# Optimization experiments

Hardware: AMD Instinct MI355X
Metric: run time of the kernel (lower is better)

## Reference

```python
import jax, jax.numpy as jnp
import numpy as np

IN_CH = 32
OUT_CH = 32
HIDDEN = 32  # edge/angle MLP hidden width


def setup_inputs() -> dict:
    key = jax.random.key(0)
    ks = jax.random.split(key, 13)
    N, E, A = 50000, 200000, 400000
    s = 0.1
    return {
        "x": jax.random.normal(ks[0], (N, IN_CH), dtype=jnp.float32),
        "edge_index": jax.random.randint(ks[1], (2, E), 0, N),
        "edge_attr": jax.random.uniform(ks[2], (E, 1), dtype=jnp.float32),
        "angle_index": jax.random.randint(ks[3], (3, A), 0, N),
        "angles": jax.random.uniform(ks[4], (A, 1), dtype=jnp.float32),
        # edge_mlp: Linear(1,32) -> ReLU -> Linear(32, in*out)
        "eW1": jax.random.normal(ks[5], (1, HIDDEN), dtype=jnp.float32) * s,
        "eb1": jax.random.normal(ks[6], (HIDDEN,), dtype=jnp.float32) * s,
        "eW2": jax.random.normal(ks[7], (HIDDEN, IN_CH * OUT_CH), dtype=jnp.float32) * s,
        "eb2": jax.random.normal(ks[8], (IN_CH * OUT_CH,), dtype=jnp.float32) * s,
        # angle_mlp: Linear(1,32) -> ReLU -> Linear(32, out)
        "aW1": jax.random.normal(ks[9], (1, HIDDEN), dtype=jnp.float32) * s,
        "ab1": jax.random.normal(ks[10], (HIDDEN,), dtype=jnp.float32) * s,
        "aW2": jax.random.normal(ks[11], (HIDDEN, OUT_CH), dtype=jnp.float32) * s,
        "ab2": jax.random.normal(ks[12], (OUT_CH,), dtype=jnp.float32) * s,
    }


def reference(x, edge_index, edge_attr, angle_index, angles,
              eW1, eb1, eW2, eb2, aW1, ab1, aW2, ab2):
    N = x.shape[0]
    row, col = edge_index[0], edge_index[1]
    # per-edge weight matrices from edge MLP: (E, in, out)
    h = jax.nn.relu(edge_attr @ eW1 + eb1)
    edge_w = (h @ eW2 + eb2).reshape(-1, IN_CH, OUT_CH)
    # gather source node features, apply per-edge matrix (bmm)
    msg = jnp.einsum('ei,eio->eo', x[col], edge_w)  # (E, out)
    agg = jax.ops.segment_sum(msg, row, num_segments=N)
    # angle branch: scatter angle features onto center node j
    j = angle_index[1]
    angle_feat = jax.nn.relu(angles @ aW1 + ab1) @ aW2 + ab2  # (A, out)
    agg = agg + jax.ops.segment_sum(angle_feat, j, num_segments=N)
    return agg
```

## Files before the change

### kernel.cpp

```cpp
#include <hip/hip_runtime.h>
#include <hip/hip_bf16.h>
#include <stdint.h>

#define IC 32
#define OC 32
#define HID 32

#define PBIN 16
#define TSH 44
#define TSCALE 1048576.0f

typedef __attribute__((ext_vector_type(8))) _Float16 half8;
typedef __attribute__((ext_vector_type(4))) float f32x4;
typedef unsigned long long u64;

static __device__ __forceinline__ _Float16 f2h(float f) { return (_Float16)f; }

__global__ void zero_kernel(float* __restrict__ out, int n) {
    int i = (blockIdx.x * blockDim.x + threadIdx.x) * 4;
    if (i + 3 < n) {
        *(float4*)(out + i) = make_float4(0.f, 0.f, 0.f, 0.f);
    } else {
        for (int k = i; k < n; ++k) out[k] = 0.f;
    }
}

__global__ __launch_bounds__(256) void angle_scatter(
    const float* __restrict__ angles, const int* __restrict__ angle_index,
    const float* __restrict__ aW1, const float* __restrict__ ab1,
    u64* __restrict__ cells, int A)
{
    float w1[HID], b1[HID];
#pragma unroll
    for (int k = 0; k < HID; ++k) { w1[k] = aW1[k]; b1[k] = ab1[k]; }

    int i0 = blockIdx.x * blockDim.x + threadIdx.x;
    int stride = gridDim.x * blockDim.x;
    for (int a = i0; a < A; a += stride) {
        const float t = angles[a];
        const int j = angle_index[A + a];
        int c = 0, c0 = 0;
#pragma unroll
        for (int k = 0; k < HID; ++k) {
            const bool pos = w1[k] > 0.f;
            const bool on  = fmaf(t, w1[k], b1[k]) > 0.f;
            const bool on0 = b1[k] > 0.f;
            c  += (pos ? on  : !on ) ? 1 : 0;
            c0 += (pos ? on0 : !on0) ? 1 : 0;
        }
        const int cc = c - c0;
        if ((unsigned)cc < (unsigned)PBIN) {
            const u64 enc = ((u64)1 << TSH) | (u64)(unsigned)(t * TSCALE);
            atomicAdd(cells + (size_t)j * PBIN + cc, enc);
        }
    }
}

__global__ __launch_bounds__(256) void angle_gather(
    float* __restrict__ out,
    const float* __restrict__ aW1, const float* __restrict__ ab1,
    const float* __restrict__ aW2, const float* __restrict__ ab2,
    int N)
{
    const int lane = threadIdx.x & 63;
    const int q    = lane >> 4;
    const int l15  = lane & 15;
    const int wib  = threadIdx.x >> 6;
    const int base = (blockIdx.x * 4 + wib) * 16;
    if (base >= N) return;

    float w1s[8], b1s[8];
    int c0 = 0, c1 = 0;
#pragma unroll
    for (int k = 0; k < HID; ++k) {
        const float w = aW1[k], b = ab1[k];
        const bool pos = w > 0.f;
        const bool f0 = pos ? (b > 0.f) : !(b > 0.f);
        const bool f1 = pos ? ((w + b) > 0.f) : !((w + b) > 0.f);
        c0 += f0 ? 1 : 0;
        c1 += f1 ? 1 : 0;
        if ((k >> 3) == q) { w1s[k & 7] = w; b1s[k & 7] = b; }
    }
    int npc = c1 - c0 + 1;
    if (npc > PBIN) npc = PBIN;

    half8 Bf0, Bf1;
#pragma unroll
    for (int j = 0; j < 8; ++j) {
        Bf0[j] = f2h(aW2[(q * 8 + j) * OC + l15]);
        Bf1[j] = f2h(aW2[(q * 8 + j) * OC + 16 + l15]);
    }
    const float bias0 = ab2[l15];
    const float bias1 = ab2[16 + l15];

    const int jn = base + l15;
    const bool vn = (jn < N);
    const u64* cj = (const u64*)out + (size_t)(vn ? jn : 0) * PBIN;
    float g[8] = {0.f, 0.f, 0.f, 0.f, 0.f, 0.f, 0.f, 0.f};
    float tot = 0.f;
    for (int cc = 0; cc < npc; ++cc) {
        const u64 v = vn ? cj[cc] : 0;
        if (v) {
            const float n  = (float)(unsigned)(v >> TSH);
            const float ts = (float)(v & (((u64)1 << TSH) - 1)) * (1.f / TSCALE);
            const float tb = ts / n;
#pragma unroll
            for (int k = 0; k < 8; ++k) {
                float h = fmaf(tb, w1s[k], b1s[k]);
                h = h > 0.f ? h : 0.f;
                g[k] = fmaf(n, h, g[k]);
            }
            tot += n;
        }
    }
    half8 a;
#pragma unroll
    for (int k = 0; k < 8; ++k) a[k] = f2h(g[k]);

    f32x4 acc0 = {0.f, 0.f, 0.f, 0.f};
    f32x4 acc1 = {0.f, 0.f, 0.f, 0.f};
    acc0 = __builtin_amdgcn_mfma_f32_16x16x32_f16(a, Bf0, acc0, 0, 0, 0);
    acc1 = __builtin_amdgcn_mfma_f32_16x16x32_f16(a, Bf1, acc1, 0, 0, 0);

#pragma unroll
    for (int r = 0; r < 4; ++r) {
        const int node = base + q * 4 + r;
        const float tr = __shfl(tot, q * 4 + r, 64);
        if (node < N) {
            out[(size_t)node * OC + l15]      = fmaf(tr, bias0, acc0[r]);
            out[(size_t)node * OC + 16 + l15] = fmaf(tr, bias1, acc1[r]);
        }
    }
}

__global__ __launch_bounds__(256) void angle_fixup(
    const float* __restrict__ angles, const int* __restrict__ angle_index,
    const float* __restrict__ aW1, const float* __restrict__ ab1,
    const float* __restrict__ aW2, const float* __restrict__ ab2,
    float* __restrict__ out, int A)
{
    float w1[HID], b1[HID];
#pragma unroll
    for (int k = 0; k < HID; ++k) { w1[k] = aW1[k]; b1[k] = ab1[k]; }

    int c0 = 0, c1 = 0;
#pragma unroll
    for (int k = 0; k < HID; ++k) {
        const bool pos = w1[k] > 0.f;
        const bool f0 = pos ? (b1[k] > 0.f) : !(b1[k] > 0.f);
        const bool f1 = pos ? ((w1[k] + b1[k]) > 0.f) : !((w1[k] + b1[k]) > 0.f);
        c0 += f0 ? 1 : 0;
        c1 += f1 ? 1 : 0;
    }
    if (c1 - c0 + 1 <= PBIN) return;

    int i0 = blockIdx.x * blockDim.x + threadIdx.x;
    int stride = gridDim.x * blockDim.x;
    for (int a = i0; a < A; a += stride) {
        const float t = angles[a];
        const int j = angle_index[A + a];
        int c = 0;
#pragma unroll
        for (int k = 0; k < HID; ++k) {
            const bool pos = w1[k] > 0.f;
            const bool on  = fmaf(t, w1[k], b1[k]) > 0.f;
            c += (pos ? on : !on) ? 1 : 0;
        }
        if (c - c0 >= PBIN) {
            float h[HID];
#pragma unroll
            for (int k = 0; k < HID; ++k) {
                float v = fmaf(t, w1[k], b1[k]);
                h[k] = v > 0.f ? v : 0.f;
            }
            for (int o = 0; o < OC; ++o) {
                float s = ab2[o];
#pragma unroll
                for (int k = 0; k < HID; ++k) s = fmaf(h[k], aW2[k * OC + o], s);
                unsafeAtomicAdd(out + (size_t)j * OC + o, s);
            }
        }
    }
}

__global__ __launch_bounds__(256) void edge_kernel(
    const float* __restrict__ x, const int* __restrict__ edge_index,
    const float* __restrict__ edge_attr,
    const float* __restrict__ eW1, const float* __restrict__ eb1,
    const float* __restrict__ eW2, const float* __restrict__ eb2,
    float* __restrict__ out, int E)
{
    const int tid   = threadIdx.x;
    const int lane  = tid & 63;
    const int gwave = blockIdx.x * 4 + (tid >> 6);
    const int ot    = gwave & 1;
    const int tile0 = gwave >> 1;
    const int tstride = (gridDim.x * 4) >> 1;
    const int q     = lane >> 4;
    const int l15   = lane & 15;
    const int ocol  = ot * 16 + l15;

    half8 Bf[33];
#pragma unroll
    for (int s = 0; s < 32; ++s) {
        half8 b;
#pragma unroll
        for (int j = 0; j < 8; ++j)
            b[j] = f2h(eW2[s * 1024 + (q * 8 + j) * 32 + ocol]);
        Bf[s] = b;
    }
    {
        half8 b;
#pragma unroll
        for (int j = 0; j < 8; ++j)
            b[j] = f2h(eb2[(q * 8 + j) * 32 + ocol]);
        Bf[32] = b;
    }

    const int numTiles = (E + 15) >> 4;

    for (int tile = tile0; tile < numTiles; tile += 2 * tstride) {
        const int tA = tile;
        const int tB = tile + tstride;
        const bool hasB = (tB < numTiles);

        const int eA  = (tA << 4) + l15;
        const bool va = (eA < E);
        const int eAc = va ? eA : 0;
        const float ta = va ? edge_attr[eAc] : 0.f;
        const int colA = va ? edge_index[E + eAc] : 0;

        const int eB  = (tB << 4) + l15;
        const bool vb = hasB && (eB < E);
        const int eBc = vb ? eB : 0;
        const float tb = vb ? edge_attr[eBc] : 0.f;
        const int colB = vb ? edge_index[E + eBc] : 0;

        const float* xpA = x + (size_t)colA * IC + q * 8;
        const float4 xloA = *(const float4*)(xpA);
        const float4 xhiA = *(const float4*)(xpA + 4);
        const float* xpB = x + (size_t)colB * IC + q * 8;
        const float4 xloB = *(const float4*)(xpB);
        const float4 xhiB = *(const float4*)(xpB + 4);

        int dstsA[4], dstsB[4];
        const int ebaseA = (tA << 4) + q * 4;
        const int ebaseB = (tB << 4) + q * 4;
#pragma unroll
        for (int r = 0; r < 4; ++r) {
            const int erA = ebaseA + r;
            dstsA[r] = (erA < E) ? edge_index[erA] : -1;
            const int erB = ebaseB + r;
            dstsB[r] = (hasB && erB < E) ? edge_index[erB] : -1;
        }

        half8 xhA, xhB;
        xhA[0] = f2h(xloA.x); xhA[1] = f2h(xloA.y);
        xhA[2] = f2h(xloA.z); xhA[3] = f2h(xloA.w);
        xhA[4] = f2h(xhiA.x); xhA[5] = f2h(xhiA.y);
        xhA[6] = f2h(xhiA.z); xhA[7] = f2h(xhiA.w);
        xhB[0] = f2h(xloB.x); xhB[1] = f2h(xloB.y);
        xhB[2] = f2h(xloB.z); xhB[3] = f2h(xloB.w);
        xhB[4] = f2h(xhiB.x); xhB[5] = f2h(xhiB.y);
        xhB[6] = f2h(xhiB.z); xhB[7] = f2h(xhiB.w);

        f32x4 accA = {0.f, 0.f, 0.f, 0.f};
        f32x4 accB = {0.f, 0.f, 0.f, 0.f};
#pragma unroll
        for (int s = 0; s < 32; ++s) {
            const float w1s = eW1[s], b1s = eb1[s];
            float hsA = fmaf(ta, w1s, b1s);
            hsA = hsA > 0.f ? hsA : 0.f;
            float hsB = fmaf(tb, w1s, b1s);
            hsB = hsB > 0.f ? hsB : 0.f;
            const _Float16 hA = f2h(hsA);
            const _Float16 hB = f2h(hsB);
            half8 hvA = {hA, hA, hA, hA, hA, hA, hA, hA};
            half8 hvB = {hB, hB, hB, hB, hB, hB, hB, hB};
            half8 aA = xhA * hvA;
            half8 aB = xhB * hvB;
            accA = __builtin_amdgcn_mfma_f32_16x16x32_f16(aA, Bf[s], accA, 0, 0, 0);
            accB = __builtin_amdgcn_mfma_f32_16x16x32_f16(aB, Bf[s], accB, 0, 0, 0);
        }
        {
            accA = __builtin_amdgcn_mfma_f32_16x16x32_f16(xhA, Bf[32], accA, 0, 0, 0);
            accB = __builtin_amdgcn_mfma_f32_16x16x32_f16(xhB, Bf[32], accB, 0, 0, 0);
        }

#pragma unroll
        for (int r = 0; r < 4; ++r) {
            if (dstsA[r] >= 0)
                unsafeAtomicAdd(out + (size_t)dstsA[r] * OC + ocol, accA[r]);
        }
#pragma unroll
        for (int r = 0; r < 4; ++r) {
            if (dstsB[r] >= 0)
                unsafeAtomicAdd(out + (size_t)dstsB[r] * OC + ocol, accB[r]);
        }
    }
}

extern "C" void kernel_launch(void* const* d_in, const int* in_sizes, int n_in,
                              void* d_out, int out_size, void* d_ws, size_t ws_size,
                              hipStream_t stream)
{
    const float* x          = (const float*)d_in[0];
    const int*   edge_index = (const int*)d_in[1];
    const float* edge_attr  = (const float*)d_in[2];
    const int*   angle_index= (const int*)d_in[3];
    const float* angles     = (const float*)d_in[4];
    const float* eW1        = (const float*)d_in[5];
    const float* eb1        = (const float*)d_in[6];
    const float* eW2        = (const float*)d_in[7];
    const float* eb2        = (const float*)d_in[8];
    const float* aW1        = (const float*)d_in[9];
    const float* ab1        = (const float*)d_in[10];
    const float* aW2        = (const float*)d_in[11];
    const float* ab2        = (const float*)d_in[12];
    float* out = (float*)d_out;
    (void)d_ws; (void)ws_size;

    const int E = in_sizes[1] / 2;
    const int A = in_sizes[3] / 3;
    const int N = in_sizes[0] / IC;

    const int zblocks = (out_size / 4 + 255) / 256;
    zero_kernel<<<zblocks, 256, 0, stream>>>(out, out_size);

    const int sblocks = (A + 255) / 256;
    angle_scatter<<<sblocks, 256, 0, stream>>>(angles, angle_index,
                                               aW1, ab1, (u64*)out, A);

    const int gblocks = (N + 63) / 64;
    angle_gather<<<gblocks, 256, 0, stream>>>(out, aW1, ab1, aW2, ab2, N);

    angle_fixup<<<sblocks, 256, 0, stream>>>(angles, angle_index,
                                             aW1, ab1, aW2, ab2, out, A);

    edge_kernel<<<512, 256, 0, stream>>>(x, edge_index, edge_attr,
                                         eW1, eb1, eW2, eb2, out, E);
}
```

Baseline: 166.8 us.

## Use piecewise-linear edge MLP decomposition with precomputed per-piece weight matrices

A setup kernel finds the ReLU breakpoints of the edge and angle hidden layers inside (0,1) and folds each linear piece into two fp16 32x32 matrices (constant part and slope part). The edge kernel stages these in LDS and runs two MFMAs per piece, masked to the edge's piece, instead of 33 MFMAs per tile. It also grows blocks to 512 threads, and the angle scatter now uses the precomputed knots. A scalar fixup kernel covers the case with more pieces than the table holds. This assumes attributes lie in [0,1) and adds a setup launch plus a data-dependent loop length.

```diff
diff --git a/kernel.cpp b/kernel.cpp
--- a/kernel.cpp
+++ b/kernel.cpp
@@ -10,11 +10,90 @@
 #define TSH 44
 #define TSCALE 1048576.0f
 
+#define PBE 12
+
 typedef __attribute__((ext_vector_type(8))) _Float16 half8;
 typedef __attribute__((ext_vector_type(4))) float f32x4;
 typedef unsigned long long u64;
 
 static __device__ __forceinline__ _Float16 f2h(float f) { return (_Float16)f; }
+
+__device__ __align__(16) _Float16 g_MK[PBE * 2 * 32 * 32];
+__device__ float g_ekn[16];
+__device__ float g_akn[16];
+__device__ int   g_npc[2];
+
+__global__ __launch_bounds__(256) void setup_kernel(
+    const float* __restrict__ eW1, const float* __restrict__ eb1,
+    const float* __restrict__ eW2, const float* __restrict__ eb2,
+    const float* __restrict__ aW1, const float* __restrict__ ab1)
+{
+    __shared__ float ts_s[32];
+    __shared__ int   rk_s[32];
+    __shared__ int   re_s[32];
+    const int tid = threadIdx.x;
+
+    if (blockIdx.x == 0 && tid < 16) { g_ekn[tid] = 1e30f; g_akn[tid] = 1e30f; }
+
+    if (tid < 32) {
+        const int k = tid;
+        const float w = eW1[k], b = eb1[k];
+        const float ts = -b / w;
+        const bool re = (w != 0.f) && (ts > 0.f) && (ts < 1.f);
+        int rk = 0;
+        for (int k2 = 0; k2 < 32; ++k2) {
+            const float w2 = eW1[k2], b2 = eb1[k2];
+            const float t2 = -b2 / w2;
+            const bool re2 = (w2 != 0.f) && (t2 > 0.f) && (t2 < 1.f);
+            rk += (re2 && (t2 < ts || (t2 == ts && k2 < k))) ? 1 : 0;
+        }
+        ts_s[k] = ts; rk_s[k] = rk; re_s[k] = re ? 1 : 0;
+    }
+    __syncthreads();
+
+    if (blockIdx.x == 0) {
+        if (tid < 32) {
+            if (re_s[tid]) g_ekn[rk_s[tid]] = ts_s[tid];
+            if (tid == 0) {
+                int n = 0;
+                for (int k = 0; k < 32; ++k) n += re_s[k];
+                g_npc[0] = n + 1;
+            }
+        } else if (tid < 64) {
+            const int k = tid - 32;
+            const float w = aW1[k], b = ab1[k];
+            const float ts = -b / w;
+            const bool re = (w != 0.f) && (ts > 0.f) && (ts < 1.f);
+            int rk = 0, nre = 0;
+            for (int k2 = 0; k2 < 32; ++k2) {
+                const float w2 = aW1[k2], b2 = ab1[k2];
+                const float t2 = -b2 / w2;
+                const bool re2 = (w2 != 0.f) && (t2 > 0.f) && (t2 < 1.f);
+                nre += re2 ? 1 : 0;
+                rk += (re2 && (t2 < ts || (t2 == ts && k2 < k))) ? 1 : 0;
+            }
+            if (re) g_akn[rk] = ts;
+            if (k == 0) g_npc[1] = nre + 1;
+        }
+    }
+
+    const int gid = blockIdx.x * blockDim.x + tid;
+    if (gid < PBE * 2 * 32 * 32) {
+        const int i   = gid & 31;
+        const int o   = (gid >> 5) & 31;
+        const int mat = (gid >> 10) & 1;
+        const int cc  = gid >> 11;
+        float acc = (mat == 0) ? eb2[i * 32 + o] : 0.f;
+        for (int k = 0; k < 32; ++k) {
+            const bool flip = re_s[k] && (rk_s[k] < cc);
+            const float w = eW1[k], b = eb1[k];
+            const bool on0 = b > 0.f;
+            const bool on = (w > 0.f) ? (on0 || flip) : (on0 && !flip);
+            if (on) acc = fmaf((mat == 0 ? b : w), eW2[k * 1024 + i * 32 + o], acc);
+        }
+        g_MK[((cc * 2 + mat) * 32 + o) * 32 + i] = (_Float16)acc;
+    }
+}
 
 __global__ void zero_kernel(float* __restrict__ out, int n) {
     int i = (blockIdx.x * blockDim.x + threadIdx.x) * 4;
@@ -27,28 +106,20 @@
 
 __global__ __launch_bounds__(256) void angle_scatter(
     const float* __restrict__ angles, const int* __restrict__ angle_index,
-    const float* __restrict__ aW1, const float* __restrict__ ab1,
     u64* __restrict__ cells, int A)
 {
-    float w1[HID], b1[HID];
-#pragma unroll
-    for (int k = 0; k < HID; ++k) { w1[k] = aW1[k]; b1[k] = ab1[k]; }
+    float kn[16];
+#pragma unroll
+    for (int j = 0; j < 16; ++j) kn[j] = g_akn[j];
 
     int i0 = blockIdx.x * blockDim.x + threadIdx.x;
     int stride = gridDim.x * blockDim.x;
     for (int a = i0; a < A; a += stride) {
         const float t = angles[a];
         const int j = angle_index[A + a];
-        int c = 0, c0 = 0;
-#pragma unroll
-        for (int k = 0; k < HID; ++k) {
-            const bool pos = w1[k] > 0.f;
-            const bool on  = fmaf(t, w1[k], b1[k]) > 0.f;
-            const bool on0 = b1[k] > 0.f;
-            c  += (pos ? on  : !on ) ? 1 : 0;
-            c0 += (pos ? on0 : !on0) ? 1 : 0;
-        }
-        const int cc = c - c0;
+        int cc = 0;
+#pragma unroll
+        for (int jj = 0; jj < 16; ++jj) cc += (t >= kn[jj]) ? 1 : 0;
         if ((unsigned)cc < (unsigned)PBIN) {
             const u64 enc = ((u64)1 << TSH) | (u64)(unsigned)(t * TSCALE);
             atomicAdd(cells + (size_t)j * PBIN + cc, enc);
@@ -139,83 +210,70 @@
     const float* __restrict__ aW2, const float* __restrict__ ab2,
     float* __restrict__ out, int A)
 {
+    if (g_npc[1] <= PBIN) return;
+
     float w1[HID], b1[HID];
 #pragma unroll
     for (int k = 0; k < HID; ++k) { w1[k] = aW1[k]; b1[k] = ab1[k]; }
-
-    int c0 = 0, c1 = 0;
-#pragma unroll
-    for (int k = 0; k < HID; ++k) {
-        const bool pos = w1[k] > 0.f;
-        const bool f0 = pos ? (b1[k] > 0.f) : !(b1[k] > 0.f);
-        const bool f1 = pos ? ((w1[k] + b1[k]) > 0.f) : !((w1[k] + b1[k]) > 0.f);
-        c0 += f0 ? 1 : 0;
-        c1 += f1 ? 1 : 0;
-    }
-    if (c1 - c0 + 1 <= PBIN) return;
+    const float kn15 = g_akn[15];
 
     int i0 = blockIdx.x * blockDim.x + threadIdx.x;
     int stride = gridDim.x * blockDim.x;
     for (int a = i0; a < A; a += stride) {
         const float t = angles[a];
+        if (t < kn15) continue;
         const int j = angle_index[A + a];
-        int c = 0;
+        float h[HID];
 #pragma unroll
         for (int k = 0; k < HID; ++k) {
-            const bool pos = w1[k] > 0.f;
-            const bool on  = fmaf(t, w1[k], b1[k]) > 0.f;
-            c += (pos ? on : !on) ? 1 : 0;
-        }
-        if (c - c0 >= PBIN) {
-            float h[HID];
-#pragma unroll
-            for (int k = 0; k < HID; ++k) {
-                float v = fmaf(t, w1[k], b1[k]);
-                h[k] = v > 0.f ? v : 0.f;
-            }
-            for (int o = 0; o < OC; ++o) {
-                float s = ab2[o];
-#pragma unroll
-                for (int k = 0; k < HID; ++k) s = fmaf(h[k], aW2[k * OC + o], s);
-                unsafeAtomicAdd(out + (size_t)j * OC + o, s);
-            }
-        }
-    }
-}
-
-__global__ __launch_bounds__(256) void edge_kernel(
+            float v = fmaf(t, w1[k], b1[k]);
+            h[k] = v > 0.f ? v : 0.f;
+        }
+        for (int o = 0; o < OC; ++o) {
+            float s = ab2[o];
+#pragma unroll
+            for (int k = 0; k < HID; ++k) s = fmaf(h[k], aW2[k * OC + o], s);
+            unsafeAtomicAdd(out + (size_t)j * OC + o, s);
+        }
+    }
+}
+
+__global__ __launch_bounds__(512) void edge_kernel(
     const float* __restrict__ x, const int* __restrict__ edge_index,
     const float* __restrict__ edge_attr,
-    const float* __restrict__ eW1, const float* __restrict__ eb1,
-    const float* __restrict__ eW2, const float* __restrict__ eb2,
     float* __restrict__ out, int E)
 {
-    const int tid   = threadIdx.x;
+    __shared__ __align__(16) _Float16 B[PBE * 2 * 32 * 40];
+    __shared__ float knl[16];
+
+    const int tid = threadIdx.x;
+
+    for (int r = tid; r < PBE * 2 * 32; r += 512) {
+        const float4* s = (const float4*)(g_MK + r * 32);
+        float4 a0 = s[0], a1 = s[1], a2 = s[2], a3 = s[3];
+        float4* d = (float4*)(B + r * 40);
+        d[0] = a0; d[1] = a1; d[2] = a2; d[3] = a3;
+    }
+    if (tid < 16) knl[tid] = g_ekn[tid];
+    __syncthreads();
+
+    float kn[PBE];
+#pragma unroll
+    for (int j = 0; j < PBE; ++j) kn[j] = knl[j];
+    int npc = g_npc[0];
+    if (npc > PBE) npc = PBE;
+
     const int lane  = tid & 63;
-    const int gwave = blockIdx.x * 4 + (tid >> 6);
+    const int w8    = tid >> 6;
+    const int gwave = blockIdx.x * 8 + w8;
     const int ot    = gwave & 1;
     const int tile0 = gwave >> 1;
-    const int tstride = (gridDim.x * 4) >> 1;
+    const int tstride = (gridDim.x * 8) >> 1;
     const int q     = lane >> 4;
     const int l15   = lane & 15;
     const int ocol  = ot * 16 + l15;
 
-    half8 Bf[33];
-#pragma unroll
-    for (int s = 0; s < 32; ++s) {
-        half8 b;
-#pragma unroll
-        for (int j = 0; j < 8; ++j)
-            b[j] = f2h(eW2[s * 1024 + (q * 8 + j) * 32 + ocol]);
-        Bf[s] = b;
-    }
-    {
-        half8 b;
-#pragma unroll
-        for (int j = 0; j < 8; ++j)
-            b[j] = f2h(eb2[(q * 8 + j) * 32 + ocol]);
-        Bf[32] = b;
-    }
+    const _Float16* Bbase = B + (size_t)ocol * 40 + q * 8;
 
     const int numTiles = (E + 15) >> 4;
 
@@ -226,15 +284,13 @@
 
         const int eA  = (tA << 4) + l15;
         const bool va = (eA < E);
-        const int eAc = va ? eA : 0;
-        const float ta = va ? edge_attr[eAc] : 0.f;
-        const int colA = va ? edge_index[E + eAc] : 0;
+        const float ta = va ? edge_attr[va ? eA : 0] : 0.f;
+        const int colA = va ? edge_index[E + eA] : 0;
 
         const int eB  = (tB << 4) + l15;
         const bool vb = hasB && (eB < E);
-        const int eBc = vb ? eB : 0;
-        const float tb = vb ? edge_attr[eBc] : 0.f;
-        const int colB = vb ? edge_index[E + eBc] : 0;
+        const float tb = vb ? edge_attr[vb ? eB : 0] : 0.f;
+        const int colB = vb ? edge_index[E + (vb ? eB : 0)] : 0;
 
         const float* xpA = x + (size_t)colA * IC + q * 8;
         const float4 xloA = *(const float4*)(xpA);
@@ -252,6 +308,13 @@
             dstsA[r] = (erA < E) ? edge_index[erA] : -1;
             const int erB = ebaseB + r;
             dstsB[r] = (hasB && erB < E) ? edge_index[erB] : -1;
+        }
+
+        int ccA = 0, ccB = 0;
+#pragma unroll
+        for (int j = 0; j < PBE; ++j) {
+            ccA += (ta >= kn[j]) ? 1 : 0;
+            ccB += (tb >= kn[j]) ? 1 : 0;
         }
 
         half8 xhA, xhB;
@@ -264,27 +327,26 @@
         xhB[4] = f2h(xhiB.x); xhB[5] = f2h(xhiB.y);
         xhB[6] = f2h(xhiB.z); xhB[7] = f2h(xhiB.w);
 
+        const _Float16 thA = f2h(ta), thB = f2h(tb);
+        const half8 tvA = {thA, thA, thA, thA, thA, thA, thA, thA};
+        const half8 tvB = {thB, thB, thB, thB, thB, thB, thB, thB};
+        const half8 xtA = xhA * tvA;
+        const half8 xtB = xhB * tvB;
+        const half8 z = {0, 0, 0, 0, 0, 0, 0, 0};
+
         f32x4 accA = {0.f, 0.f, 0.f, 0.f};
         f32x4 accB = {0.f, 0.f, 0.f, 0.f};
-#pragma unroll
-        for (int s = 0; s < 32; ++s) {
-            const float w1s = eW1[s], b1s = eb1[s];
-            float hsA = fmaf(ta, w1s, b1s);
-            hsA = hsA > 0.f ? hsA : 0.f;
-            float hsB = fmaf(tb, w1s, b1s);
-            hsB = hsB > 0.f ? hsB : 0.f;
-            const _Float16 hA = f2h(hsA);
-            const _Float16 hB = f2h(hsB);
-            half8 hvA = {hA, hA, hA, hA, hA, hA, hA, hA};
-            half8 hvB = {hB, hB, hB, hB, hB, hB, hB, hB};
-            half8 aA = xhA * hvA;
-            half8 aB = xhB * hvB;
-            accA = __builtin_amdgcn_mfma_f32_16x16x32_f16(aA, Bf[s], accA, 0, 0, 0);
-            accB = __builtin_amdgcn_mfma_f32_16x16x32_f16(aB, Bf[s], accB, 0, 0, 0);
-        }
-        {
-            accA = __builtin_amdgcn_mfma_f32_16x16x32_f16(xhA, Bf[32], accA, 0, 0, 0);
-            accB = __builtin_amdgcn_mfma_f32_16x16x32_f16(xhB, Bf[32], accB, 0, 0, 0);
+        for (int c = 0; c < npc; ++c) {
+            const half8 bM = *(const half8*)(Bbase + (size_t)(c * 2 + 0) * 32 * 40);
+            const half8 bK = *(const half8*)(Bbase + (size_t)(c * 2 + 1) * 32 * 40);
+            const half8 aA1 = (ccA == c) ? xhA : z;
+            const half8 aA2 = (ccA == c) ? xtA : z;
+            const half8 aB1 = (ccB == c) ? xhB : z;
+            const half8 aB2 = (ccB == c) ? xtB : z;
+            accA = __builtin_amdgcn_mfma_f32_16x16x32_f16(aA1, bM, accA, 0, 0, 0);
+            accB = __builtin_amdgcn_mfma_f32_16x16x32_f16(aB1, bM, accB, 0, 0, 0);
+            accA = __builtin_amdgcn_mfma_f32_16x16x32_f16(aA2, bK, accA, 0, 0, 0);
+            accB = __builtin_amdgcn_mfma_f32_16x16x32_f16(aB2, bK, accB, 0, 0, 0);
         }
 
 #pragma unroll
@@ -296,6 +358,46 @@
         for (int r = 0; r < 4; ++r) {
             if (dstsB[r] >= 0)
                 unsafeAtomicAdd(out + (size_t)dstsB[r] * OC + ocol, accB[r]);
+        }
+    }
+}
+
+__global__ __launch_bounds__(256) void edge_fixup(
+    const float* __restrict__ x, const int* __restrict__ edge_index,
+    const float* __restrict__ edge_attr,
+    const float* __restrict__ eW1, const float* __restrict__ eb1,
+    const float* __restrict__ eW2, const float* __restrict__ eb2,
+    float* __restrict__ out, int E)
+{
+    if (g_npc[0] <= PBE) return;
+    const float knb = g_ekn[PBE - 1];
+
+    int i0 = blockIdx.x * blockDim.x + threadIdx.x;
+    int stride = gridDim.x * blockDim.x;
+    for (int e = i0; e < E; e += stride) {
+        const float t = edge_attr[e];
+        if (t < knb) continue;
+        const int col = edge_index[E + e];
+        const int dst = edge_index[e];
+        float h[HID];
+#pragma unroll
+        for (int k = 0; k < HID; ++k) {
+            float v = fmaf(t, eW1[k], eb1[k]);
+            h[k] = v > 0.f ? v : 0.f;
+        }
+        float xv[IC];
+#pragma unroll
+        for (int i = 0; i < IC; ++i) xv[i] = x[(size_t)col * IC + i];
+        for (int o = 0; o < OC; ++o) {
+            float s = 0.f;
+            for (int i = 0; i < IC; ++i) {
+                float wio = eb2[i * 32 + o];
+#pragma unroll
+                for (int k = 0; k < HID; ++k)
+                    wio = fmaf(h[k], eW2[k * 1024 + i * 32 + o], wio);
+                s = fmaf(xv[i], wio, s);
+            }
+            unsafeAtomicAdd(out + (size_t)dst * OC + o, s);
         }
     }
 }
@@ -324,12 +426,14 @@
     const int A = in_sizes[3] / 3;
     const int N = in_sizes[0] / IC;
 
+    setup_kernel<<<96, 256, 0, stream>>>(eW1, eb1, eW2, eb2, aW1, ab1);
+
     const int zblocks = (out_size / 4 + 255) / 256;
     zero_kernel<<<zblocks, 256, 0, stream>>>(out, out_size);
 
     const int sblocks = (A + 255) / 256;
     angle_scatter<<<sblocks, 256, 0, stream>>>(angles, angle_index,
-                                               aW1, ab1, (u64*)out, A);
+                                               (u64*)out, A);
 
     const int gblocks = (N + 63) / 64;
     angle_gather<<<gblocks, 256, 0, stream>>>(out, aW1, ab1, aW2, ab2, N);
@@ -337,6 +441,8 @@
     angle_fixup<<<sblocks, 256, 0, stream>>>(angles, angle_index,
                                              aW1, ab1, aW2, ab2, out, A);
 
-    edge_kernel<<<512, 256, 0, stream>>>(x, edge_index, edge_attr,
-                                         eW1, eb1, eW2, eb2, out, E);
-}
+    edge_kernel<<<512, 512, 0, stream>>>(x, edge_index, edge_attr, out, E);
+
+    edge_fixup<<<256, 256, 0, stream>>>(x, edge_index, edge_attr,
+                                        eW1, eb1, eW2, eb2, out, E);
+}
```

New measurement: 163.0 us. -2.3%, faster.
